# Performance work log

Hardware: AMD Instinct MI355X
Metric: run time of the kernel (lower is better)

## Reference

```python
import jax, jax.numpy as jnp
import numpy as np

H_HEADS = 8
EPS = 1e-5

def layernorm(x, g, b):
    m = jnp.mean(x, axis=-1, keepdims=True)
    v = jnp.mean(jnp.square(x - m), axis=-1, keepdims=True)
    return (x - m) * jax.lax.rsqrt(v + EPS) * g + b

def setup_inputs() -> dict:
    key = jax.random.key(0)
    ks = jax.random.split(key, 8)
    B, H, W, C = 8, 64, 64, 256
    C2 = 2 * C
    s = lambda n: 1.0 / np.sqrt(n)
    return {
        "x1": jax.random.normal(ks[0], (B, H, W, C), jnp.float32),
        "x2": jax.random.normal(ks[1], (B, H, W, C), jnp.float32),
        "norm1_g": jnp.ones((C,)), "norm1_b": jnp.zeros((C,)),
        "lin_w": jax.random.normal(ks[2], (C, C), jnp.float32) * s(C),
        "lin_b": jnp.zeros((C,)),
        "reproj_w": jax.random.normal(ks[3], (C, C), jnp.float32) * s(C),
        "reproj_b": jnp.zeros((C,)),
        "attn_norm_g": jnp.ones((C,)), "attn_norm_b": jnp.zeros((C,)),
        "norm2_g": jnp.ones((C,)), "norm2_b": jnp.zeros((C,)),
        "fc1_w": jax.random.normal(ks[4], (C2, C), jnp.float32) * s(C),
        "fc1_b": jnp.zeros((C2,)),
        "dw_w": jax.random.normal(ks[5], (C2, 1, 3, 3), jnp.float32) * s(9),
        "dw_b": jnp.zeros((C2,)),
        "ffn_n1_g": jnp.ones((C2,)), "ffn_n1_b": jnp.zeros((C2,)),
        "fc2_w": jax.random.normal(ks[6], (C, C2), jnp.float32) * s(C2),
        "fc2_b": jnp.zeros((C,)),
        "ffn_n3_g": jnp.ones((C,)), "ffn_n3_b": jnp.zeros((C,)),
    }

def reference(x1, x2, norm1_g, norm1_b, lin_w, lin_b, reproj_w, reproj_b,
              attn_norm_g, attn_norm_b, norm2_g, norm2_b, fc1_w, fc1_b,
              dw_w, dw_b, ffn_n1_g, ffn_n1_b, fc2_w, fc2_b, ffn_n3_g, ffn_n3_b):
    B, H, W, C = x1.shape
    N = H * W
    h = H_HEADS
    dk = C // h  # head key channels; value_dim == key_dim == C here
    # shared norm1 + linear projection of both streams
    n1 = layernorm(x1, norm1_g, norm1_b) @ lin_w.T + lin_b  # (B,H,W,C) queries src
    n2 = layernorm(x2, norm1_g, norm1_b) @ lin_w.T + lin_b  # (B,H,W,C) key/value src
    # (B,N,C) -> (B,h,d,N); channel dim split contiguously per head (matches torch slicing)
    q = jnp.transpose(n1.reshape(B, N, h, dk), (0, 2, 3, 1))
    k = jnp.transpose(n2.reshape(B, N, h, dk), (0, 2, 3, 1))
    v = k  # values are the same tensor slices (value_dim == key_dim)
    k = jax.nn.softmax(k, axis=-1)   # softmax over tokens N
    q = jax.nn.softmax(q, axis=2)    # softmax over head channel dim
    # linear attention: context (B,h,dk,dv), then project back to tokens
    context = jnp.einsum('bhdn,bhvn->bhdv', k, v)
    att = jnp.einsum('bhdv,bhdn->bhvn', context, q)  # (B,h,dv,N)
    agg = att.reshape(B, C, H, W)
    # 1x1 conv reprojection (value_channels -> key_channels)
    rep = jnp.einsum('bvhw,kv->bhwk', agg, reproj_w) + reproj_b  # (B,H,W,C)
    attn_out = layernorm(rep, attn_norm_g, attn_norm_b)
    # out_proj is Identity since key_dim == in_dim
    tx = attn_out + x1
    y = layernorm(tx, norm2_g, norm2_b)  # skip_ffn input
    # skip_ffn
    h1 = y @ fc1_w.T + fc1_b  # (B,H,W,2C)
    hc = jnp.transpose(h1, (0, 3, 1, 2))  # NCHW
    dw = jax.lax.conv_general_dilated(
        hc, dw_w, window_strides=(1, 1), padding='SAME',
        dimension_numbers=('NCHW', 'OIHW', 'NCHW'),
        feature_group_count=hc.shape[1])
    dw = jnp.transpose(dw + dw_b[None, :, None, None], (0, 2, 3, 1))  # NHWC
    ax = jax.nn.gelu(layernorm(dw, ffn_n1_g, ffn_n1_b), approximate=False)
    out = ax @ fc2_w.T + fc2_b
    return layernorm(out + y, ffn_n3_g, ffn_n3_b)
```

## Files before the change

### kernel.cpp

```cpp
#include <hip/hip_runtime.h>

#define BTOK 32768
#define CC 256
#define CC2 512
#define NBATCH 8

typedef __bf16 bf16x8 __attribute__((ext_vector_type(8)));
typedef float f32x4 __attribute__((ext_vector_type(4)));
typedef unsigned short u16x8 __attribute__((ext_vector_type(8)));
typedef unsigned short u16x4 __attribute__((ext_vector_type(4)));

__device__ __forceinline__ float b2f(unsigned short u) {
    return __uint_as_float(((unsigned)u) << 16);
}
__device__ __forceinline__ unsigned short f2b(float f) {
    unsigned x = __float_as_uint(f);
    return (unsigned short)((x + 0x7fffu + ((x >> 16) & 1u)) >> 16);
}
__device__ __forceinline__ float wredsum(float v) {
#pragma unroll
    for (int m = 1; m < 64; m <<= 1) v += __shfl_xor(v, m);
    return v;
}
__device__ __forceinline__ float grp4sum(float v) {
    v += __shfl_xor(v, 1);
    v += __shfl_xor(v, 2);
    return v;
}

typedef __attribute__((address_space(3))) unsigned int lds_u32;
typedef const __attribute__((address_space(1))) unsigned int glb_u32;
__device__ __forceinline__ void gload_lds16(const unsigned short* g, unsigned short* l) {
    __builtin_amdgcn_global_load_lds((glb_u32*)g, (lds_u32*)l, 16, 0, 0);
}

__global__ __launch_bounds__(256) void probe_kernel(
    const unsigned short* __restrict__ x, int* __restrict__ flag)
{
    int t = threadIdx.x;
    int c = 0;
    for (int i = t; i < 1024; i += 256) {
        unsigned e = (x[i] >> 7) & 0xFFu;
        c += (e >= 110u && e <= 135u) ? 1 : 0;
    }
#pragma unroll
    for (int m = 1; m < 64; m <<= 1) c += __shfl_xor(c, m);
    __shared__ int acc[4];
    if ((t & 63) == 0) acc[t >> 6] = c;
    __syncthreads();
    if (t == 0) *flag = ((acc[0] + acc[1] + acc[2] + acc[3]) >= 896) ? 1 : 0;
}

__global__ __launch_bounds__(256) void cvt_params_kernel(
    const int* __restrict__ flagp,
    const void* p0, const void* p1, const void* p2, const void* p3, const void* p4,
    const void* p5, const void* p6, const void* p7, const void* p8, const void* p9,
    const void* p10, const void* p11, const void* p12, const void* p13, const void* p14,
    const void* p15, const void* p16, const void* p17, const void* p18, const void* p19,
    unsigned short* __restrict__ dst)
{
    bool isb = (*flagp != 0);
    long g = (long)blockIdx.x * 256 + threadIdx.x;
    long str = (long)gridDim.x * 256;
#define CVT(src, off, n)                                                        \
    for (long i = g; i < (long)(n); i += str)                                   \
        dst[(off) + i] = isb ? ((const unsigned short*)(src))[i]                \
                             : f2b(((const float*)(src))[i]);
    CVT(p0, 0, 256)
    CVT(p1, 256, 256)
    CVT(p2, 512, 65536)
    CVT(p3, 66048, 256)
    CVT(p4, 66304, 65536)
    CVT(p5, 131840, 256)
    CVT(p6, 132096, 256)
    CVT(p7, 132352, 256)
    CVT(p8, 132608, 256)
    CVT(p9, 132864, 256)
    CVT(p10, 133120, 131072)
    CVT(p11, 264192, 512)
    CVT(p12, 264704, 4608)
    CVT(p13, 269312, 512)
    CVT(p14, 269824, 512)
    CVT(p15, 270336, 512)
    CVT(p16, 270848, 131072)
    CVT(p17, 401920, 256)
    CVT(p18, 402176, 256)
    CVT(p19, 402432, 256)
#undef CVT
}

__global__ __launch_bounds__(256) void dw_transpose_kernel(
    const void* __restrict__ src, unsigned short* __restrict__ dwt,
    const int* __restrict__ flagp)
{
    bool isb = (*flagp != 0);
    for (int i = threadIdx.x; i < 4608; i += 256) {
        int tap = i >> 9, c = i & 511;
        dwt[i] = isb ? ((const unsigned short*)src)[c * 9 + tap]
                     : f2b(((const float*)src)[c * 9 + tap]);
    }
}

__global__ __launch_bounds__(256) void ln_dual_kernel(
    const void* __restrict__ x1, const void* __restrict__ x2,
    const unsigned short* __restrict__ g, const unsigned short* __restrict__ b,
    unsigned short* __restrict__ out, const int* __restrict__ flagp)
{
    bool isb = (*flagp != 0);
    int wid = threadIdx.x >> 6, l = threadIdx.x & 63;
    long row = (long)blockIdx.x * 4 + wid;
    const void* xsel = (row < BTOK) ? x1 : x2;
    long r = (row < BTOK) ? row : (row - BTOK);
    float f[4];
    if (isb) {
        u16x4 v = *reinterpret_cast<const u16x4*>((const unsigned short*)xsel + r * CC + l * 4);
#pragma unroll
        for (int j = 0; j < 4; j++) f[j] = b2f(v[j]);
    } else {
        f32x4 v = *reinterpret_cast<const f32x4*>((const float*)xsel + r * CC + l * 4);
#pragma unroll
        for (int j = 0; j < 4; j++) f[j] = v[j];
    }
    float mean = wredsum(f[0] + f[1] + f[2] + f[3]) * (1.f / CC);
    float d[4], sq = 0.f;
#pragma unroll
    for (int j = 0; j < 4; j++) { d[j] = f[j] - mean; sq += d[j] * d[j]; }
    float rs = rsqrtf(wredsum(sq) * (1.f / CC) + 1e-5f);
    u16x4 gv = *reinterpret_cast<const u16x4*>(g + l * 4);
    u16x4 bv = *reinterpret_cast<const u16x4*>(b + l * 4);
    u16x4 o;
#pragma unroll
    for (int j = 0; j < 4; j++) o[j] = f2b(d[j] * rs * b2f(gv[j]) + b2f(bv[j]));
    *reinterpret_cast<u16x4*>(out + row * CC + l * 4) = o;
}

template<int K>
__global__ __launch_bounds__(256) void gemm_lds_kernel(
    const unsigned short* __restrict__ A, const unsigned short* __restrict__ Wt,
    const unsigned short* __restrict__ bias, unsigned short* __restrict__ out,
    int O, int nwg)
{
    __shared__ unsigned short Asm[2][4096];
    __shared__ unsigned short Bsm[2][4096];
    int t = threadIdx.x, l = t & 63, w = t >> 6;
    int bid = blockIdx.x, cpx = nwg >> 3;
    int wg = (bid & 7) * cpx + (bid >> 3);
    int ntn = O >> 7;
    long tm = (long)(wg / ntn) << 7;
    int tn = (wg % ntn) << 7;
    int wr = (w >> 1) << 6, wc = (w & 1) << 6;

    int rloc = t >> 2;
    int q = (t & 3) ^ ((t >> 3) & 3);
    const unsigned short* ga0 = A + (tm + rloc) * K + q * 8;
    const unsigned short* ga1 = ga0 + (long)64 * K;
    const unsigned short* gb0 = Wt + (long)(tn + rloc) * K + q * 8;
    const unsigned short* gb1 = gb0 + (long)64 * K;

    int rr = l & 15;
    int sA = ((l >> 4) ^ ((rr >> 1) & 3)) << 3;
    int aoff[4], boff[4];
#pragma unroll
    for (int m = 0; m < 4; m++) aoff[m] = (wr + m * 16 + rr) * 32 + sA;
#pragma unroll
    for (int n = 0; n < 4; n++) boff[n] = (wc + n * 16 + rr) * 32 + sA;

    f32x4 acc[4][4];
#pragma unroll
    for (int m = 0; m < 4; m++)
#pragma unroll
        for (int n = 0; n < 4; n++) acc[m][n] = {0.f, 0.f, 0.f, 0.f};

    auto stage = [&](int buf, int koff) {
        gload_lds16(ga0 + koff, &Asm[buf][w * 512]);
        gload_lds16(ga1 + koff, &Asm[buf][2048 + w * 512]);
        gload_lds16(gb0 + koff, &Bsm[buf][w * 512]);
        gload_lds16(gb1 + koff, &Bsm[buf][2048 + w * 512]);
    };
    auto compute = [&](int buf) {
        bf16x8 af[4], bfr[4];
#pragma unroll
        for (int m = 0; m < 4; m++) af[m] = *reinterpret_cast<const bf16x8*>(&Asm[buf][aoff[m]]);
#pragma unroll
        for (int n = 0; n < 4; n++) bfr[n] = *reinterpret_cast<const bf16x8*>(&Bsm[buf][boff[n]]);
#pragma unroll
        for (int m = 0; m < 4; m++)
#pragma unroll
            for (int n = 0; n < 4; n++)
                acc[m][n] = __builtin_amdgcn_mfma_f32_16x16x32_bf16(af[m], bfr[n], acc[m][n], 0, 0, 0);
    };

    stage(0, 0);
    asm volatile("s_waitcnt vmcnt(0)" ::: "memory");
    __syncthreads();
    constexpr int NK = K / 32;
#pragma unroll
    for (int kt = 0; kt < NK; kt += 2) {
        if (kt + 1 < NK) stage(1, (kt + 1) * 32);
        compute(0);
        asm volatile("s_waitcnt vmcnt(0)" ::: "memory");
        __syncthreads();
        if (kt + 1 < NK) {
            if (kt + 2 < NK) stage(0, (kt + 2) * 32);
            compute(1);
            asm volatile("s_waitcnt vmcnt(0)" ::: "memory");
            __syncthreads();
        }
    }

    int orow = (l >> 4) << 2;
    int ocol = l & 15;
    float bi[4];
#pragma unroll
    for (int n = 0; n < 4; n++) bi[n] = b2f(bias[tn + wc + n * 16 + ocol]);
#pragma unroll
    for (int m = 0; m < 4; m++) {
#pragma unroll
        for (int n = 0; n < 4; n++) {
#pragma unroll
            for (int j = 0; j < 4; j++) {
                out[(tm + wr + m * 16 + orow + j) * O + tn + wc + n * 16 + ocol] =
                    f2b(acc[m][n][j] + bi[n]);
            }
        }
    }
}

#define REPS 272
template<int K, int MODE>
__global__ __launch_bounds__(512) void gemm_fused_kernel(
    const unsigned short* __restrict__ A, const unsigned short* __restrict__ Wt,
    const unsigned short* __restrict__ bias, const void* __restrict__ xin,
    const unsigned short* __restrict__ g1, const unsigned short* __restrict__ b1,
    const unsigned short* __restrict__ g2p, const unsigned short* __restrict__ b2p,
    void* __restrict__ outp, const int* __restrict__ flagp, int nwg)
{
    __shared__ unsigned short SA[2][4096];
    __shared__ unsigned short SB[2][8192];
    __shared__ unsigned short Rep[128 * REPS];
    int t = threadIdx.x, l = t & 63, w = t >> 6;
    int bid = blockIdx.x, cpx = nwg >> 3;
    int wg = (bid & 7) * cpx + (bid >> 3);
    long tm = (long)wg << 7;
    int wr = (w >> 2) << 6, wc = (w & 3) << 6;

    int rloc = t >> 2;
    int q = (t & 3) ^ ((t >> 3) & 3);
    const unsigned short* ga0 = A + (tm + rloc) * K + q * 8;
    const unsigned short* gb0 = Wt + (long)rloc * K + q * 8;
    const unsigned short* gb1 = gb0 + (long)128 * K;

    int rr = l & 15;
    int sA = ((l >> 4) ^ ((rr >> 1) & 3)) << 3;
    int aoff[4], boff[4];
#pragma unroll
    for (int m = 0; m < 4; m++) aoff[m] = (wr + m * 16 + rr) * 32 + sA;
#pragma unroll
    for (int n = 0; n < 4; n++) boff[n] = (wc + n * 16 + rr) * 32 + sA;

    f32x4 acc[4][4];
#pragma unroll
    for (int m = 0; m < 4; m++)
#pragma unroll
        for (int n = 0; n < 4; n++) acc[m][n] = {0.f, 0.f, 0.f, 0.f};

    auto stage = [&](int buf, int koff) {
        gload_lds16(ga0 + koff, &SA[buf][w * 512]);
        gload_lds16(gb0 + koff, &SB[buf][w * 512]);
        gload_lds16(gb1 + koff, &SB[buf][4096 + w * 512]);
    };
    auto compute = [&](int buf) {
        bf16x8 af[4], bfr[4];
#pragma unroll
        for (int m = 0; m < 4; m++) af[m] = *reinterpret_cast<const bf16x8*>(&SA[buf][aoff[m]]);
#pragma unroll
        for (int n = 0; n < 4; n++) bfr[n] = *reinterpret_cast<const bf16x8*>(&SB[buf][boff[n]]);
#pragma unroll
        for (int m = 0; m < 4; m++)
#pragma unroll
            for (int n = 0; n < 4; n++)
                acc[m][n] = __builtin_amdgcn_mfma_f32_16x16x32_bf16(af[m], bfr[n], acc[m][n], 0, 0, 0);
    };

    stage(0, 0);
    asm volatile("s_waitcnt vmcnt(0)" ::: "memory");
    __syncthreads();
    constexpr int NK = K / 32;
#pragma unroll
    for (int kt = 0; kt < NK; kt += 2) {
        if (kt + 1 < NK) stage(1, (kt + 1) * 32);
        compute(0);
        asm volatile("s_waitcnt vmcnt(0)" ::: "memory");
        __syncthreads();
        if (kt + 1 < NK) {
            if (kt + 2 < NK) stage(0, (kt + 2) * 32);
            compute(1);
            asm volatile("s_waitcnt vmcnt(0)" ::: "memory");
            __syncthreads();
        }
    }

    int orow = (l >> 4) << 2, ocol = l & 15;
#pragma unroll
    for (int n = 0; n < 4; n++) {
        float bi = b2f(bias[wc + n * 16 + ocol]);
#pragma unroll
        for (int m = 0; m < 4; m++)
#pragma unroll
            for (int j = 0; j < 4; j++)
                Rep[(wr + m * 16 + orow + j) * REPS + wc + n * 16 + ocol] =
                    f2b(acc[m][n][j] + bi);
    }
    __syncthreads();

    bool isb = (*flagp != 0);
    int r = t >> 2, qd = t & 3;
    long grow = tm + r;
    const unsigned short* rrow = Rep + r * REPS + qd * 8;
    u16x8 rv[8];
#pragma unroll
    for (int i = 0; i < 8; i++) rv[i] = *reinterpret_cast<const u16x8*>(rrow + i * 32);

    if constexpr (MODE == 0) {
        float s1 = 0.f;
#pragma unroll
        for (int i = 0; i < 8; i++)
#pragma unroll
            for (int j = 0; j < 8; j++) s1 += b2f(rv[i][j]);
        s1 = grp4sum(s1);
        float mean = s1 * (1.f / 256);
        float s2 = 0.f;
#pragma unroll
        for (int i = 0; i < 8; i++)
#pragma unroll
            for (int j = 0; j < 8; j++) { float d = b2f(rv[i][j]) - mean; s2 += d * d; }
        s2 = grp4sum(s2);
        float rs = rsqrtf(s2 * (1.f / 256) + 1e-5f);
        const float* xf = (const float*)xin + grow * 256 + qd * 8;
        const unsigned short* xb = (const unsigned short*)xin + grow * 256 + qd * 8;
        float tt[8][8];
        float t1 = 0.f, t2 = 0.f;
#pragma unroll
        for (int i = 0; i < 8; i++) {
            int cb = qd * 8 + i * 32;
            u16x8 gg = *reinterpret_cast<const u16x8*>(g1 + cb);
            u16x8 bb = *reinterpret_cast<const u16x8*>(b1 + cb);
            float xv[8];
            if (isb) {
                u16x8 x8 = *reinterpret_cast<const u16x8*>(xb + i * 32);
#pragma unroll
                for (int j = 0; j < 8; j++) xv[j] = b2f(x8[j]);
            } else {
                f32x4 a0 = *reinterpret_cast<const f32x4*>(xf + i * 32);
                f32x4 a1 = *reinterpret_cast<const f32x4*>(xf + i * 32 + 4);
#pragma unroll
                for (int j = 0; j < 4; j++) { xv[j] = a0[j]; xv[4 + j] = a1[j]; }
            }
#pragma unroll
            for (int j = 0; j < 8; j++) {
                float nv = (b2f(rv[i][j]) - mean) * rs * b2f(gg[j]) + b2f(bb[j]);
                float v = nv + xv[j];
                tt[i][j] = v;
                t1 += v; t2 += v * v;
            }
        }
        t1 = grp4sum(t1); t2 = grp4sum(t2);
        float mean2 = t1 * (1.f / 256);
        float rs2 = rsqrtf(t2 * (1.f / 256) - mean2 * mean2 + 1e-5f);
        unsigned short* ob = (unsigned short*)outp + grow * 256 + qd * 8;
#pragma unroll
        for (int i = 0; i < 8; i++) {
            int cb = qd * 8 + i * 32;
            u16x8 g2v = *reinterpret_cast<const u16x8*>(g2p + cb);
            u16x8 b2vv = *reinterpret_cast<const u16x8*>(b2p + cb);
            u16x8 o;
#pragma unroll
            for (int j = 0; j < 8; j++)
                o[j] = f2b((tt[i][j] - mean2) * rs2 * b2f(g2v[j]) + b2f(b2vv[j]));
            *reinterpret_cast<u16x8*>(ob + i * 32) = o;
        }
    } else {
        const unsigned short* yb = (const unsigned short*)xin + grow * 256 + qd * 8;
        u16x8 yv[8];
#pragma unroll
        for (int i = 0; i < 8; i++) yv[i] = *reinterpret_cast<const u16x8*>(yb + i * 32);
        float t1 = 0.f, t2 = 0.f;
#pragma unroll
        for (int i = 0; i < 8; i++)
#pragma unroll
            for (int j = 0; j < 8; j++) {
                float tt = b2f(rv[i][j]) + b2f(yv[i][j]);
                t1 += tt; t2 += tt * tt;
            }
        t1 = grp4sum(t1); t2 = grp4sum(t2);
        float mean2 = t1 * (1.f / 256);
        float rs2 = rsqrtf(t2 * (1.f / 256) - mean2 * mean2 + 1e-5f);
        float* of = (float*)outp + grow * 256 + qd * 8;
        unsigned short* ob = (unsigned short*)outp + grow * 256 + qd * 8;
#pragma unroll
        for (int i = 0; i < 8; i++) {
            int cb = qd * 8 + i * 32;
            u16x8 gg = *reinterpret_cast<const u16x8*>(g1 + cb);
            u16x8 bb = *reinterpret_cast<const u16x8*>(b1 + cb);
            float rvals[8];
#pragma unroll
            for (int j = 0; j < 8; j++) {
                float tt = b2f(rv[i][j]) + b2f(yv[i][j]);
                rvals[j] = (tt - mean2) * rs2 * b2f(gg[j]) + b2f(bb[j]);
            }
            if (isb) {
                u16x8 o;
#pragma unroll
                for (int j = 0; j < 8; j++) o[j] = f2b(rvals[j]);
                *reinterpret_cast<u16x8*>(ob + i * 32) = o;
            } else {
                f32x4 o0, o1;
#pragma unroll
                for (int j = 0; j < 4; j++) { o0[j] = rvals[j]; o1[j] = rvals[4 + j]; }
                *reinterpret_cast<f32x4*>(of + i * 32) = o0;
                *reinterpret_cast<f32x4*>(of + i * 32 + 4) = o1;
            }
        }
    }
}

__global__ __launch_bounds__(256) void ctx_part_kernel(
    const unsigned short* __restrict__ n2, float* __restrict__ pctx,
    float* __restrict__ pcs)
{
    int blk = blockIdx.x;
    int b = blk >> 7, hd = (blk >> 4) & 7, slab = blk & 15;
    int t = threadIdx.x;
    __shared__ float ld[32][33], eld[32][33];
    int d = t >> 3;
    int v0 = (t & 7) << 2;
    int ln_ = t >> 3;
    int lc = (t & 7) << 2;
    f32x4 acc = {0.f, 0.f, 0.f, 0.f};
    float se = 0.f;
    const unsigned short* base = n2 + ((long)b * 4096 + slab * 256) * CC + hd * 32;
    for (int n0 = 0; n0 < 256; n0 += 32) {
        u16x4 rv = *reinterpret_cast<const u16x4*>(base + (long)(n0 + ln_) * CC + lc);
#pragma unroll
        for (int j = 0; j < 4; j++) {
            float x = b2f(rv[j]);
            ld[ln_][lc + j] = x;
            eld[ln_][lc + j] = __expf(x);
        }
        __syncthreads();
#pragma unroll 4
        for (int nn = 0; nn < 32; nn++) {
            float e = eld[nn][d];
            se += e;
#pragma unroll
            for (int j = 0; j < 4; j++) acc[j] += e * ld[nn][v0 + j];
        }
        __syncthreads();
    }
    long o = ((long)slab * NBATCH * 8 + (long)b * 8 + hd) * 1024 + (long)d * 32 + v0;
#pragma unroll
    for (int j = 0; j < 4; j++) pctx[o + j] = acc[j];
    if ((t & 7) == 0)
        pcs[(long)slab * (NBATCH * 8 * 32) + ((long)(b * 8 + hd) << 5) + d] = se;
}

__global__ __launch_bounds__(256) void ctx_reduce_kernel(
    const float* __restrict__ pctx, const float* __restrict__ pcs,
    float* __restrict__ ctx)
{
    long i = (long)blockIdx.x * 256 + threadIdx.x;
    int bh = (int)(i >> 10);
    int d = (int)((i >> 5) & 31);
    float s = 0.f, ps = 0.f;
#pragma unroll
    for (int sl = 0; sl < 16; sl++) {
        s += pctx[(long)sl * 65536 + i];
        ps += pcs[(long)sl * (NBATCH * 8 * 32) + (bh << 5) + d];
    }
    ctx[i] = s / ps;
}

__global__ __launch_bounds__(256) void att_kernel(
    const unsigned short* __restrict__ n1, const float* __restrict__ ctx,
    unsigned short* __restrict__ attv)
{
    __shared__ float cl[32 * 256];
    int b = blockIdx.x >> 6, grp = blockIdx.x & 63;
    int t = threadIdx.x, wid = t >> 6, l = t & 63;
    const float* cb = ctx + (long)b * 8192;
    for (int i = 0; i < 32; i++) {
        int gidx = t + (i << 8);
        int hd_ = gidx >> 10, dd = (gidx >> 5) & 31, vv = gidx & 31;
        cl[dd * 256 + hd_ * 32 + vv] = cb[gidx];
    }
    __syncthreads();
    int base_lane = l & 56;
    long tokbase = (long)b * 4096 + grp * 64 + wid * 16;
    const f32x4* c4 = reinterpret_cast<const f32x4*>(cl);
    for (int it = 0; it < 16; it++) {
        long tok = tokbase + it;
        u16x4 rv = *reinterpret_cast<const u16x4*>(n1 + tok * CC + l * 4);
        float x[4];
#pragma unroll
        for (int j = 0; j < 4; j++) x[j] = b2f(rv[j]);
        float mx = fmaxf(fmaxf(x[0], x[1]), fmaxf(x[2], x[3]));
        mx = fmaxf(mx, __shfl_xor(mx, 1));
        mx = fmaxf(mx, __shfl_xor(mx, 2));
        mx = fmaxf(mx, __shfl_xor(mx, 4));
        float e[4], s = 0.f;
#pragma unroll
        for (int j = 0; j < 4; j++) { e[j] = __expf(x[j] - mx); s += e[j]; }
        s += __shfl_xor(s, 1);
        s += __shfl_xor(s, 2);
        s += __shfl_xor(s, 4);
        float inv = 1.f / s;
        f32x4 o = {0.f, 0.f, 0.f, 0.f};
#pragma unroll
        for (int dd = 0; dd < 32; dd++) {
            float qv = __shfl(e[dd & 3], base_lane + (dd >> 2));
            o += qv * c4[dd * 64 + l];
        }
        o *= inv;
        u16x4 ov;
#pragma unroll
        for (int j = 0; j < 4; j++) ov[j] = f2b(o[j]);
        *reinterpret_cast<u16x4*>(attv + tok * CC + l * 4) = ov;
    }
}

__global__ __launch_bounds__(256) void dw_kernel(
    const unsigned short* __restrict__ h1, const unsigned short* __restrict__ dwt,
    const unsigned short* __restrict__ dwb, const unsigned short* __restrict__ g,
    const unsigned short* __restrict__ bb, unsigned short* __restrict__ ax)
{
    int wid = threadIdx.x >> 6, l = threadIdx.x & 63;
    int pix = blockIdx.x * 4 + wid;
    int b = pix >> 12, rem = pix & 4095, py = rem >> 6, px = rem & 63;
    int c0 = l * 8;
    u16x8 wv[9];
#pragma unroll
    for (int tap = 0; tap < 9; tap++)
        wv[tap] = *reinterpret_cast<const u16x8*>(dwt + tap * CC2 + c0);
    u16x8 biasv = *reinterpret_cast<const u16x8*>(dwb + c0);
    float acc[8];
#pragma unroll
    for (int j = 0; j < 8; j++) acc[j] = b2f(biasv[j]);
#pragma unroll
    for (int ky = 0; ky < 3; ky++) {
        int ys = py + ky - 1;
        if ((unsigned)ys >= 64u) continue;
#pragma unroll
        for (int kx = 0; kx < 3; kx++) {
            int xs = px + kx - 1;
            if ((unsigned)xs >= 64u) continue;
            u16x8 pv = *reinterpret_cast<const u16x8*>(
                h1 + ((long)(b << 12) + (ys << 6) + xs) * CC2 + c0);
            int tap = ky * 3 + kx;
#pragma unroll
            for (int j = 0; j < 8; j++)
                acc[j] += b2f(pv[j]) * b2f(wv[tap][j]);
        }
    }
    float s = 0.f;
#pragma unroll
    for (int j = 0; j < 8; j++) s += acc[j];
    float mean = wredsum(s) * (1.f / CC2);
    float d[8], sq = 0.f;
#pragma unroll
    for (int j = 0; j < 8; j++) { d[j] = acc[j] - mean; sq += d[j] * d[j]; }
    float rs = rsqrtf(wredsum(sq) * (1.f / CC2) + 1e-5f);
    u16x8 gv = *reinterpret_cast<const u16x8*>(g + c0);
    u16x8 bv = *reinterpret_cast<const u16x8*>(bb + c0);
    u16x8 o;
#pragma unroll
    for (int j = 0; j < 8; j++) {
        float nv = d[j] * rs * b2f(gv[j]) + b2f(bv[j]);
        o[j] = f2b(0.5f * nv * (1.f + erff(nv * 0.70710678118654752f)));
    }
    *reinterpret_cast<u16x8*>(ax + (long)pix * CC2 + c0) = o;
}

extern "C" void kernel_launch(void* const* d_in, const int* in_sizes, int n_in,
                              void* d_out, int out_size, void* d_ws, size_t ws_size,
                              hipStream_t stream)
{
    char* w = (char*)d_ws;
    const size_t S1B = (size_t)BTOK * CC * 2;
    const size_t STATSB = (size_t)(2 * NBATCH * CC + NBATCH * 8 * 32 * 32) * 4;
    const size_t PARAMS_ELEMS = 402688 + 4608;
    const size_t need = 6 * S1B + STATSB + 64 + PARAMS_ELEMS * 2;
    if (ws_size < need) return;

    unsigned short* ln12 = (unsigned short*)w;
    unsigned short* n12  = (unsigned short*)(w + 2 * S1B);
    unsigned short* nn1  = n12;
    unsigned short* nn2  = n12 + (size_t)BTOK * CC;
    unsigned short* attv = ln12;
    unsigned short* ybuf = nn1;
    unsigned short* h1   = ln12;
    unsigned short* axb  = (unsigned short*)(w + 4 * S1B);
    float* pctx = (float*)(w + 4 * S1B + (2048 << 10));
    float* pcs  = (float*)(w + 4 * S1B + (2048 << 10) + (4 << 20));
    float* ctxb = (float*)(w + 6 * S1B) + 2 * NBATCH * CC;
    int*   flag = (int*)(w + 6 * S1B + STATSB);
    unsigned short* pb = (unsigned short*)(w + 6 * S1B + STATSB + 64);

    unsigned short* n1g  = pb + 0;
    unsigned short* n1b  = pb + 256;
    unsigned short* linw = pb + 512;
    unsigned short* linb = pb + 66048;
    unsigned short* repw = pb + 66304;
    unsigned short* repb = pb + 131840;
    unsigned short* ang  = pb + 132096;
    unsigned short* anb  = pb + 132352;
    unsigned short* g2   = pb + 132608;
    unsigned short* b2v  = pb + 132864;
    unsigned short* fc1w = pb + 133120;
    unsigned short* fc1b = pb + 264192;
    unsigned short* dwb  = pb + 269312;
    unsigned short* fn1g = pb + 269824;
    unsigned short* fn1b = pb + 270336;
    unsigned short* fc2w = pb + 270848;
    unsigned short* fc2b = pb + 401920;
    unsigned short* fn3g = pb + 402176;
    unsigned short* fn3b = pb + 402432;
    unsigned short* dwt  = pb + 402688;

    probe_kernel<<<1, 256, 0, stream>>>((const unsigned short*)d_in[0], flag);
    cvt_params_kernel<<<512, 256, 0, stream>>>(flag,
        d_in[2], d_in[3], d_in[4], d_in[5], d_in[6], d_in[7], d_in[8], d_in[9],
        d_in[10], d_in[11], d_in[12], d_in[13], d_in[14], d_in[15], d_in[16],
        d_in[17], d_in[18], d_in[19], d_in[20], d_in[21], pb);
    dw_transpose_kernel<<<1, 256, 0, stream>>>(d_in[14], dwt, flag);
    ln_dual_kernel<<<2 * BTOK / 4, 256, 0, stream>>>(d_in[0], d_in[1], n1g, n1b, ln12, flag);
    {
        int nwg = (2 * BTOK / 128) * (CC / 128);
        gemm_lds_kernel<256><<<nwg, 256, 0, stream>>>(ln12, linw, linb, n12, CC, nwg);
    }
    ctx_part_kernel<<<NBATCH * 8 * 16, 256, 0, stream>>>(nn2, pctx, pcs);
    ctx_reduce_kernel<<<256, 256, 0, stream>>>(pctx, pcs, ctxb);
    att_kernel<<<NBATCH * 64, 256, 0, stream>>>(nn1, ctxb, attv);
    {
        int nwg = BTOK / 128;
        gemm_fused_kernel<256, 0><<<nwg, 512, 0, stream>>>(
            attv, repw, repb, d_in[0], ang, anb, g2, b2v, ybuf, flag, nwg);
    }
    {
        int nwg = (BTOK / 128) * (CC2 / 128);
        gemm_lds_kernel<256><<<nwg, 256, 0, stream>>>(ybuf, fc1w, fc1b, h1, CC2, nwg);
    }
    dw_kernel<<<BTOK / 4, 256, 0, stream>>>(h1, dwt, dwb, fn1g, fn1b, axb);
    {
        int nwg = BTOK / 128;
        gemm_fused_kernel<512, 1><<<nwg, 512, 0, stream>>>(
            axb, fc2w, fc2b, ybuf, fn3g, fn3b, fn3g, fn3b, d_out, flag, nwg);
    }
}
```

Baseline: 204.7 us.

## Fold attention context into reprojection weights and fuse query softmax into projection GEMM

Removes att_kernel by computing a per-batch matrix M = reproj_w · context^T (ctx2m_kernel), so the reprojection GEMM multiplies the softmaxed queries by M directly instead of reading an intermediate attention tensor. The per-head query softmax is moved into the epilogue of the first projection GEMM for the x1 half, using 16-lane shuffles. The fused GEMM gets a three-stage LDS pipeline that keeps two loads in flight, and the dw weight transpose is folded into the parameter conversion kernel, saving a launch. In exchange the reprojection weight becomes per-batch, LDS use grows, and bf16 rounding of M adds error.

```diff
diff --git a/kernel.cpp b/kernel.cpp
--- a/kernel.cpp
+++ b/kernel.cpp
@@ -78,7 +78,11 @@
     CVT(p9, 132864, 256)
     CVT(p10, 133120, 131072)
     CVT(p11, 264192, 512)
-    CVT(p12, 264704, 4608)
+    for (long i = g; i < 4608; i += str) {
+        int tap = (int)(i >> 9), c = (int)(i & 511);
+        dst[264704 + i] = isb ? ((const unsigned short*)p12)[c * 9 + tap]
+                              : f2b(((const float*)p12)[c * 9 + tap]);
+    }
     CVT(p13, 269312, 512)
     CVT(p14, 269824, 512)
     CVT(p15, 270336, 512)
@@ -89,18 +93,6 @@
 #undef CVT
 }
 
-__global__ __launch_bounds__(256) void dw_transpose_kernel(
-    const void* __restrict__ src, unsigned short* __restrict__ dwt,
-    const int* __restrict__ flagp)
-{
-    bool isb = (*flagp != 0);
-    for (int i = threadIdx.x; i < 4608; i += 256) {
-        int tap = i >> 9, c = i & 511;
-        dwt[i] = isb ? ((const unsigned short*)src)[c * 9 + tap]
-                     : f2b(((const float*)src)[c * 9 + tap]);
-    }
-}
-
 __global__ __launch_bounds__(256) void ln_dual_kernel(
     const void* __restrict__ x1, const void* __restrict__ x2,
     const unsigned short* __restrict__ g, const unsigned short* __restrict__ b,
@@ -134,7 +126,7 @@
     *reinterpret_cast<u16x4*>(out + row * CC + l * 4) = o;
 }
 
-template<int K>
+template<int K, bool QSM>
 __global__ __launch_bounds__(256) void gemm_lds_kernel(
     const unsigned short* __restrict__ A, const unsigned short* __restrict__ Wt,
     const unsigned short* __restrict__ bias, unsigned short* __restrict__ out,
@@ -213,6 +205,38 @@
     float bi[4];
 #pragma unroll
     for (int n = 0; n < 4; n++) bi[n] = b2f(bias[tn + wc + n * 16 + ocol]);
+
+    if constexpr (QSM) {
+        if (tm < (long)BTOK) {
+#pragma unroll
+            for (int P = 0; P < 2; P++) {
+#pragma unroll
+                for (int m = 0; m < 4; m++) {
+#pragma unroll
+                    for (int j = 0; j < 4; j++) {
+                        float v0 = acc[m][2 * P][j] + bi[2 * P];
+                        float v1 = acc[m][2 * P + 1][j] + bi[2 * P + 1];
+                        float mx = fmaxf(v0, v1);
+                        mx = fmaxf(mx, __shfl_xor(mx, 1));
+                        mx = fmaxf(mx, __shfl_xor(mx, 2));
+                        mx = fmaxf(mx, __shfl_xor(mx, 4));
+                        mx = fmaxf(mx, __shfl_xor(mx, 8));
+                        float e0 = __expf(v0 - mx), e1 = __expf(v1 - mx);
+                        float s = e0 + e1;
+                        s += __shfl_xor(s, 1);
+                        s += __shfl_xor(s, 2);
+                        s += __shfl_xor(s, 4);
+                        s += __shfl_xor(s, 8);
+                        float inv = 1.f / s;
+                        long rowb = (tm + wr + m * 16 + orow + j) * O + tn + wc + ocol;
+                        out[rowb + (2 * P) * 16] = f2b(e0 * inv);
+                        out[rowb + (2 * P + 1) * 16] = f2b(e1 * inv);
+                    }
+                }
+            }
+            return;
+        }
+    }
 #pragma unroll
     for (int m = 0; m < 4; m++) {
 #pragma unroll
@@ -235,14 +259,16 @@
     const unsigned short* __restrict__ g2p, const unsigned short* __restrict__ b2p,
     void* __restrict__ outp, const int* __restrict__ flagp, int nwg)
 {
-    __shared__ unsigned short SA[2][4096];
-    __shared__ unsigned short SB[2][8192];
+    __shared__ unsigned short SA[3][4096];
+    __shared__ unsigned short SB[3][8192];
     __shared__ unsigned short Rep[128 * REPS];
     int t = threadIdx.x, l = t & 63, w = t >> 6;
     int bid = blockIdx.x, cpx = nwg >> 3;
     int wg = (bid & 7) * cpx + (bid >> 3);
     long tm = (long)wg << 7;
     int wr = (w >> 2) << 6, wc = (w & 3) << 6;
+
+    if constexpr (MODE == 0) Wt += ((tm >> 12) << 16);
 
     int rloc = t >> 2;
     int q = (t & 3) ^ ((t >> 3) & 3);
@@ -282,20 +308,18 @@
                 acc[m][n] = __builtin_amdgcn_mfma_f32_16x16x32_bf16(af[m], bfr[n], acc[m][n], 0, 0, 0);
     };
 
+    constexpr int NK = K / 32;
     stage(0, 0);
-    asm volatile("s_waitcnt vmcnt(0)" ::: "memory");
+    stage(1, 32);
+    asm volatile("s_waitcnt vmcnt(3)" ::: "memory");
     __syncthreads();
-    constexpr int NK = K / 32;
-#pragma unroll
-    for (int kt = 0; kt < NK; kt += 2) {
-        if (kt + 1 < NK) stage(1, (kt + 1) * 32);
-        compute(0);
-        asm volatile("s_waitcnt vmcnt(0)" ::: "memory");
-        __syncthreads();
+#pragma unroll
+    for (int kt = 0; kt < NK; kt++) {
+        if (kt + 2 < NK) stage((kt + 2) % 3, (kt + 2) * 32);
+        compute(kt % 3);
         if (kt + 1 < NK) {
-            if (kt + 2 < NK) stage(0, (kt + 2) * 32);
-            compute(1);
-            asm volatile("s_waitcnt vmcnt(0)" ::: "memory");
+            if (kt + 2 < NK) asm volatile("s_waitcnt vmcnt(3)" ::: "memory");
+            else             asm volatile("s_waitcnt vmcnt(0)" ::: "memory");
             __syncthreads();
         }
     }
@@ -480,51 +504,31 @@
     ctx[i] = s / ps;
 }
 
-__global__ __launch_bounds__(256) void att_kernel(
-    const unsigned short* __restrict__ n1, const float* __restrict__ ctx,
-    unsigned short* __restrict__ attv)
-{
-    __shared__ float cl[32 * 256];
-    int b = blockIdx.x >> 6, grp = blockIdx.x & 63;
-    int t = threadIdx.x, wid = t >> 6, l = t & 63;
-    const float* cb = ctx + (long)b * 8192;
-    for (int i = 0; i < 32; i++) {
-        int gidx = t + (i << 8);
-        int hd_ = gidx >> 10, dd = (gidx >> 5) & 31, vv = gidx & 31;
-        cl[dd * 256 + hd_ * 32 + vv] = cb[gidx];
-    }
-    __syncthreads();
-    int base_lane = l & 56;
-    long tokbase = (long)b * 4096 + grp * 64 + wid * 16;
-    const f32x4* c4 = reinterpret_cast<const f32x4*>(cl);
-    for (int it = 0; it < 16; it++) {
-        long tok = tokbase + it;
-        u16x4 rv = *reinterpret_cast<const u16x4*>(n1 + tok * CC + l * 4);
-        float x[4];
-#pragma unroll
-        for (int j = 0; j < 4; j++) x[j] = b2f(rv[j]);
-        float mx = fmaxf(fmaxf(x[0], x[1]), fmaxf(x[2], x[3]));
-        mx = fmaxf(mx, __shfl_xor(mx, 1));
-        mx = fmaxf(mx, __shfl_xor(mx, 2));
-        mx = fmaxf(mx, __shfl_xor(mx, 4));
-        float e[4], s = 0.f;
-#pragma unroll
-        for (int j = 0; j < 4; j++) { e[j] = __expf(x[j] - mx); s += e[j]; }
-        s += __shfl_xor(s, 1);
-        s += __shfl_xor(s, 2);
-        s += __shfl_xor(s, 4);
-        float inv = 1.f / s;
-        f32x4 o = {0.f, 0.f, 0.f, 0.f};
-#pragma unroll
-        for (int dd = 0; dd < 32; dd++) {
-            float qv = __shfl(e[dd & 3], base_lane + (dd >> 2));
-            o += qv * c4[dd * 64 + l];
-        }
-        o *= inv;
-        u16x4 ov;
-#pragma unroll
-        for (int j = 0; j < 4; j++) ov[j] = f2b(o[j]);
-        *reinterpret_cast<u16x4*>(attv + tok * CC + l * 4) = ov;
+__global__ __launch_bounds__(256) void ctx2m_kernel(
+    const float* __restrict__ ctx, const unsigned short* __restrict__ repw,
+    unsigned short* __restrict__ M)
+{
+    int b = blockIdx.x >> 3, og = blockIdx.x & 7;
+    int t = threadIdx.x;
+    int o = og * 32 + (t >> 3);
+    int hd = t & 7;
+    float wv[32];
+    const unsigned short* wr_ = repw + (long)o * 256 + hd * 32;
+#pragma unroll
+    for (int i = 0; i < 4; i++) {
+        u16x8 w8 = *reinterpret_cast<const u16x8*>(wr_ + i * 8);
+#pragma unroll
+        for (int j = 0; j < 8; j++) wv[i * 8 + j] = b2f(w8[j]);
+    }
+    const float* cb = ctx + ((long)(b * 8 + hd)) * 1024;
+    unsigned short* mb = M + ((long)b << 16) + (long)o * 256 + hd * 32;
+#pragma unroll 4
+    for (int d = 0; d < 32; d++) {
+        const float* cd = cb + d * 32;
+        float s = 0.f;
+#pragma unroll
+        for (int vv = 0; vv < 32; vv++) s += wv[vv] * cd[vv];
+        mb[d] = f2b(s);
     }
 }
 
@@ -587,7 +591,7 @@
     char* w = (char*)d_ws;
     const size_t S1B = (size_t)BTOK * CC * 2;
     const size_t STATSB = (size_t)(2 * NBATCH * CC + NBATCH * 8 * 32 * 32) * 4;
-    const size_t PARAMS_ELEMS = 402688 + 4608;
+    const size_t PARAMS_ELEMS = 402688;
     const size_t need = 6 * S1B + STATSB + 64 + PARAMS_ELEMS * 2;
     if (ws_size < need) return;
 
@@ -595,12 +599,12 @@
     unsigned short* n12  = (unsigned short*)(w + 2 * S1B);
     unsigned short* nn1  = n12;
     unsigned short* nn2  = n12 + (size_t)BTOK * CC;
-    unsigned short* attv = ln12;
     unsigned short* ybuf = nn1;
     unsigned short* h1   = ln12;
     unsigned short* axb  = (unsigned short*)(w + 4 * S1B);
     float* pctx = (float*)(w + 4 * S1B + (2048 << 10));
     float* pcs  = (float*)(w + 4 * S1B + (2048 << 10) + (4 << 20));
+    unsigned short* Mbuf = (unsigned short*)(pcs + 32768);
     float* ctxb = (float*)(w + 6 * S1B) + 2 * NBATCH * CC;
     int*   flag = (int*)(w + 6 * S1B + STATSB);
     unsigned short* pb = (unsigned short*)(w + 6 * S1B + STATSB + 64);
@@ -617,6 +621,7 @@
     unsigned short* b2v  = pb + 132864;
     unsigned short* fc1w = pb + 133120;
     unsigned short* fc1b = pb + 264192;
+    unsigned short* dwt  = pb + 264704;
     unsigned short* dwb  = pb + 269312;
     unsigned short* fn1g = pb + 269824;
     unsigned short* fn1b = pb + 270336;
@@ -624,30 +629,28 @@
     unsigned short* fc2b = pb + 401920;
     unsigned short* fn3g = pb + 402176;
     unsigned short* fn3b = pb + 402432;
-    unsigned short* dwt  = pb + 402688;
 
     probe_kernel<<<1, 256, 0, stream>>>((const unsigned short*)d_in[0], flag);
     cvt_params_kernel<<<512, 256, 0, stream>>>(flag,
         d_in[2], d_in[3], d_in[4], d_in[5], d_in[6], d_in[7], d_in[8], d_in[9],
         d_in[10], d_in[11], d_in[12], d_in[13], d_in[14], d_in[15], d_in[16],
         d_in[17], d_in[18], d_in[19], d_in[20], d_in[21], pb);
-    dw_transpose_kernel<<<1, 256, 0, stream>>>(d_in[14], dwt, flag);
     ln_dual_kernel<<<2 * BTOK / 4, 256, 0, stream>>>(d_in[0], d_in[1], n1g, n1b, ln12, flag);
     {
         int nwg = (2 * BTOK / 128) * (CC / 128);
-        gemm_lds_kernel<256><<<nwg, 256, 0, stream>>>(ln12, linw, linb, n12, CC, nwg);
+        gemm_lds_kernel<256, true><<<nwg, 256, 0, stream>>>(ln12, linw, linb, n12, CC, nwg);
     }
     ctx_part_kernel<<<NBATCH * 8 * 16, 256, 0, stream>>>(nn2, pctx, pcs);
     ctx_reduce_kernel<<<256, 256, 0, stream>>>(pctx, pcs, ctxb);
-    att_kernel<<<NBATCH * 64, 256, 0, stream>>>(nn1, ctxb, attv);
+    ctx2m_kernel<<<NBATCH * 8, 256, 0, stream>>>(ctxb, repw, Mbuf);
     {
         int nwg = BTOK / 128;
         gemm_fused_kernel<256, 0><<<nwg, 512, 0, stream>>>(
-            attv, repw, repb, d_in[0], ang, anb, g2, b2v, ybuf, flag, nwg);
+            nn1, Mbuf, repb, d_in[0], ang, anb, g2, b2v, ybuf, flag, nwg);
     }
     {
         int nwg = (BTOK / 128) * (CC2 / 128);
-        gemm_lds_kernel<256><<<nwg, 256, 0, stream>>>(ybuf, fc1w, fc1b, h1, CC2, nwg);
+        gemm_lds_kernel<256, false><<<nwg, 256, 0, stream>>>(ybuf, fc1w, fc1b, h1, CC2, nwg);
     }
     dw_kernel<<<BTOK / 4, 256, 0, stream>>>(h1, dwt, dwb, fn1g, fn1b, axb);
     {
```

After: 224.3 us. 9.6% more time.

## Triple-buffer fused GEMM K-loop and fold dw weight transpose into param conversion

Applied to the files above, without the earlier changes.

The fused reprojection GEMM moves from a double-buffered LDS pipeline to a three-stage ring. Each iteration waits only until the older stage has landed (vmcnt(3)) rather than draining every outstanding load, and it uses a bare s_barrier. Separately, the depthwise-weight transpose now runs inside the parameter-conversion kernel, which removes one tiny kernel launch. The extra LDS buffers raise shared memory per block, which may lower occupancy. The relaxed wait counts also rely on an exact count of outstanding loads per stage.

```diff
diff --git a/kernel.cpp b/kernel.cpp
--- a/kernel.cpp
+++ b/kernel.cpp
@@ -78,7 +78,11 @@
     CVT(p9, 132864, 256)
     CVT(p10, 133120, 131072)
     CVT(p11, 264192, 512)
-    CVT(p12, 264704, 4608)
+    for (long i = g; i < 4608; i += str) {
+        int tap = (int)(i >> 9), c = (int)(i & 511);
+        dst[264704 + i] = isb ? ((const unsigned short*)p12)[c * 9 + tap]
+                              : f2b(((const float*)p12)[c * 9 + tap]);
+    }
     CVT(p13, 269312, 512)
     CVT(p14, 269824, 512)
     CVT(p15, 270336, 512)
@@ -87,18 +91,6 @@
     CVT(p18, 402176, 256)
     CVT(p19, 402432, 256)
 #undef CVT
-}
-
-__global__ __launch_bounds__(256) void dw_transpose_kernel(
-    const void* __restrict__ src, unsigned short* __restrict__ dwt,
-    const int* __restrict__ flagp)
-{
-    bool isb = (*flagp != 0);
-    for (int i = threadIdx.x; i < 4608; i += 256) {
-        int tap = i >> 9, c = i & 511;
-        dwt[i] = isb ? ((const unsigned short*)src)[c * 9 + tap]
-                     : f2b(((const float*)src)[c * 9 + tap]);
-    }
 }
 
 __global__ __launch_bounds__(256) void ln_dual_kernel(
@@ -235,8 +227,8 @@
     const unsigned short* __restrict__ g2p, const unsigned short* __restrict__ b2p,
     void* __restrict__ outp, const int* __restrict__ flagp, int nwg)
 {
-    __shared__ unsigned short SA[2][4096];
-    __shared__ unsigned short SB[2][8192];
+    __shared__ unsigned short SA[3][4096];
+    __shared__ unsigned short SB[3][8192];
     __shared__ unsigned short Rep[128 * REPS];
     int t = threadIdx.x, l = t & 63, w = t >> 6;
     int bid = blockIdx.x, cpx = nwg >> 3;
@@ -282,21 +274,21 @@
                 acc[m][n] = __builtin_amdgcn_mfma_f32_16x16x32_bf16(af[m], bfr[n], acc[m][n], 0, 0, 0);
     };
 
+    constexpr int NK = K / 32;
     stage(0, 0);
-    asm volatile("s_waitcnt vmcnt(0)" ::: "memory");
-    __syncthreads();
-    constexpr int NK = K / 32;
-#pragma unroll
-    for (int kt = 0; kt < NK; kt += 2) {
-        if (kt + 1 < NK) stage(1, (kt + 1) * 32);
-        compute(0);
-        asm volatile("s_waitcnt vmcnt(0)" ::: "memory");
-        __syncthreads();
+    stage(1, 32);
+    asm volatile("s_waitcnt vmcnt(3)" ::: "memory");
+    __builtin_amdgcn_s_barrier();
+    asm volatile("" ::: "memory");
+#pragma unroll
+    for (int kt = 0; kt < NK; kt++) {
+        if (kt + 2 < NK) stage((kt + 2) % 3, (kt + 2) * 32);
+        compute(kt % 3);
         if (kt + 1 < NK) {
-            if (kt + 2 < NK) stage(0, (kt + 2) * 32);
-            compute(1);
-            asm volatile("s_waitcnt vmcnt(0)" ::: "memory");
-            __syncthreads();
+            if (kt + 2 < NK) asm volatile("s_waitcnt vmcnt(3)" ::: "memory");
+            else             asm volatile("s_waitcnt vmcnt(0)" ::: "memory");
+            __builtin_amdgcn_s_barrier();
+            asm volatile("" ::: "memory");
         }
     }
 
@@ -587,7 +579,7 @@
     char* w = (char*)d_ws;
     const size_t S1B = (size_t)BTOK * CC * 2;
     const size_t STATSB = (size_t)(2 * NBATCH * CC + NBATCH * 8 * 32 * 32) * 4;
-    const size_t PARAMS_ELEMS = 402688 + 4608;
+    const size_t PARAMS_ELEMS = 402688;
     const size_t need = 6 * S1B + STATSB + 64 + PARAMS_ELEMS * 2;
     if (ws_size < need) return;
 
@@ -617,6 +609,7 @@
     unsigned short* b2v  = pb + 132864;
     unsigned short* fc1w = pb + 133120;
     unsigned short* fc1b = pb + 264192;
+    unsigned short* dwt  = pb + 264704;
     unsigned short* dwb  = pb + 269312;
     unsigned short* fn1g = pb + 269824;
     unsigned short* fn1b = pb + 270336;
@@ -624,14 +617,12 @@
     unsigned short* fc2b = pb + 401920;
     unsigned short* fn3g = pb + 402176;
     unsigned short* fn3b = pb + 402432;
-    unsigned short* dwt  = pb + 402688;
 
     probe_kernel<<<1, 256, 0, stream>>>((const unsigned short*)d_in[0], flag);
     cvt_params_kernel<<<512, 256, 0, stream>>>(flag,
         d_in[2], d_in[3], d_in[4], d_in[5], d_in[6], d_in[7], d_in[8], d_in[9],
         d_in[10], d_in[11], d_in[12], d_in[13], d_in[14], d_in[15], d_in[16],
         d_in[17], d_in[18], d_in[19], d_in[20], d_in[21], pb);
-    dw_transpose_kernel<<<1, 256, 0, stream>>>(d_in[14], dwt, flag);
     ln_dual_kernel<<<2 * BTOK / 4, 256, 0, stream>>>(d_in[0], d_in[1], n1g, n1b, ln12, flag);
     {
         int nwg = (2 * BTOK / 128) * (CC / 128);
```

Result: faster. 195.8 us (-4.4%).
